# Kernel optimization log

Measured on AMD Instinct MI355X. Metric: run time of the kernel, lower is better.

The kernel has to match this reference:

```python
import jax, jax.numpy as jnp
import numpy as np

BLOCK_SIZE = 64
N_EMBD = 128
N_HEAD = 4
HEAD_DIM = N_EMBD // N_HEAD  # 32


def setup_inputs() -> dict:
    key = jax.random.key(0)
    kx, kq, kk, kv = jax.random.split(key, 4)
    B, T = 4096, 64
    x = jax.random.normal(kx, (B, T, N_EMBD), dtype=jnp.float32)
    # nn.Linear(n_embd, head_dim, bias=False): stored as [out,in] in torch,
    # here kept as [in, out] = [128, 32] so projection is x @ W.
    s = 1.0 / np.sqrt(N_EMBD)
    Wq = jax.random.uniform(kq, (N_EMBD, HEAD_DIM), jnp.float32, -s, s)
    Wk = jax.random.uniform(kk, (N_EMBD, HEAD_DIM), jnp.float32, -s, s)
    Wv = jax.random.uniform(kv, (N_EMBD, HEAD_DIM), jnp.float32, -s, s)
    return {"x": x, "Wq": Wq, "Wk": Wk, "Wv": Wv}


def reference(x, Wq, Wk, Wv):
    B, T, C = x.shape
    q = x @ Wq  # [B, T, Hd]
    k = x @ Wk
    v = x @ Wv
    scale = 1.0 / jnp.sqrt(jnp.asarray(k.shape[-1], x.dtype))
    wei = jnp.einsum("btd,bsd->bts", q, k) * scale  # [B, T, T]
    causal = jnp.tril(jnp.ones((T, T), dtype=bool))
    wei = jnp.where(causal, wei, -jnp.inf)
    wei = jax.nn.softmax(wei, axis=-1)
    out = jnp.einsum("bts,bsd->btd", wei, v)  # [B, T, Hd]
    return out
```

## Files before the change

kernel.cpp:

```cpp
#include <hip/hip_runtime.h>


#define TT 64
#define CC 128
#define HD 32

typedef __bf16 bf16_t;
typedef __bf16 bf8_t __attribute__((ext_vector_type(8)));
typedef __bf16 bf4_t __attribute__((ext_vector_type(4)));
typedef float  f4_t  __attribute__((ext_vector_type(4)));

__global__ __launch_bounds__(256) void prep_weights(
    const float* __restrict__ Wq, const float* __restrict__ Wk,
    const float* __restrict__ Wv, bf16_t* __restrict__ wf)
{
  int t = blockIdx.x * 256 + threadIdx.x;
  int j    = t & 7;
  int lane = (t >> 3) & 63;
  int kt   = (t >> 9) & 3;
  int n6   = t >> 11;
  int k    = kt * 32 + (lane >> 4) * 8 + j;
  int col  = (n6 & 1) * 16 + (lane & 15);
  const float* W = (n6 >> 1) == 0 ? Wq : ((n6 >> 1) == 1 ? Wk : Wv);
  wf[t] = (bf16_t)W[k * HD + col];
}

__global__ __launch_bounds__(256) void head_fused(
    const float* __restrict__ x, const bf8_t* __restrict__ wf,
    float* __restrict__ out)
{
  __shared__ __align__(16) bf16_t xs[TT][136];
  __shared__ __align__(16) bf16_t qs[TT][40];
  __shared__ __align__(16) bf16_t ks[TT][40];
  __shared__ __align__(16) bf16_t vt[HD][72];

  const int tid  = threadIdx.x;
  const int wave = tid >> 6;
  const int lane = tid & 63;
  const int quad = lane >> 4;
  const int l16  = lane & 15;
  const int b    = blockIdx.x;

  const float4* x4 = (const float4*)(x + (size_t)b * (TT * CC));
  #pragma unroll
  for (int i = 0; i < 8; ++i) {
    int e = tid + i * 256;
    float4 f = x4[e];
    int fi = e << 2;
    int row = fi >> 7, col = fi & 127;
    bf4_t h = { (bf16_t)f.x, (bf16_t)f.y, (bf16_t)f.z, (bf16_t)f.w };
    *(bf4_t*)&xs[row][col] = h;
  }
  __syncthreads();

  f4_t zero4 = {0.f, 0.f, 0.f, 0.f};
  f4_t acc[6];
  #pragma unroll
  for (int n = 0; n < 6; ++n) acc[n] = zero4;
  #pragma unroll
  for (int kk = 0; kk < 4; ++kk) {
    int k0 = kk * 32 + quad * 8;
    bf8_t a = *(const bf8_t*)&xs[wave * 16 + l16][k0];
    #pragma unroll
    for (int n = 0; n < 6; ++n) {
      bf8_t bb = wf[(n * 4 + kk) * 64 + lane];
      acc[n] = __builtin_amdgcn_mfma_f32_16x16x32_bf16(a, bb, acc[n], 0, 0, 0);
    }
  }
  #pragma unroll
  for (int r = 0; r < 4; ++r) {
    int row = wave * 16 + quad * 4 + r;
    qs[row][l16]      = (bf16_t)acc[0][r];
    qs[row][16 + l16] = (bf16_t)acc[1][r];
    ks[row][l16]      = (bf16_t)acc[2][r];
    ks[row][16 + l16] = (bf16_t)acc[3][r];
    vt[l16][row]      = (bf16_t)acc[4][r];
    vt[16 + l16][row] = (bf16_t)acc[5][r];
  }
  __syncthreads();

  bf16_t (*ps)[72] = (bf16_t(*)[72])&xs[0][0];
  f4_t sc[4];
  #pragma unroll
  for (int nt = 0; nt < 4; ++nt) sc[nt] = zero4;
  {
    bf8_t aq = *(const bf8_t*)&qs[wave * 16 + l16][quad * 8];
    #pragma unroll
    for (int nt = 0; nt < 4; ++nt) {
      if (nt <= wave) {
        bf8_t bk = *(const bf8_t*)&ks[nt * 16 + l16][quad * 8];
        sc[nt] = __builtin_amdgcn_mfma_f32_16x16x32_bf16(aq, bk, zero4, 0, 0, 0);
      }
    }
  }
  const float scale = 0.17677669529663687f;
  #pragma unroll
  for (int r = 0; r < 4; ++r) {
    int rl = quad * 4 + r;
    float vals[4];
    float vmax = -INFINITY;
    #pragma unroll
    for (int nt = 0; nt < 4; ++nt) {
      float v_ = -INFINITY;
      if (nt < wave)                         v_ = sc[nt][r] * scale;
      else if (nt == wave && l16 <= rl)      v_ = sc[nt][r] * scale;
      vals[nt] = v_;
      vmax = fmaxf(vmax, v_);
    }
    #pragma unroll
    for (int off = 1; off < 16; off <<= 1)
      vmax = fmaxf(vmax, __shfl_xor(vmax, off));
    float psum = 0.f;
    #pragma unroll
    for (int nt = 0; nt < 4; ++nt) {
      float p = (vals[nt] == -INFINITY) ? 0.f : __expf(vals[nt] - vmax);
      vals[nt] = p;
      psum += p;
    }
    #pragma unroll
    for (int off = 1; off < 16; off <<= 1)
      psum += __shfl_xor(psum, off);
    float inv = 1.0f / psum;
    int row = wave * 16 + rl;
    #pragma unroll
    for (int nt = 0; nt < 4; ++nt)
      ps[row][nt * 16 + l16] = (bf16_t)(vals[nt] * inv);
  }
  __syncthreads();

  f4_t o0 = zero4, o1 = zero4;
  #pragma unroll
  for (int kk = 0; kk < 2; ++kk) {
    int k0 = kk * 32 + quad * 8;
    bf8_t ap  = *(const bf8_t*)&ps[wave * 16 + l16][k0];
    bf8_t bv0 = *(const bf8_t*)&vt[l16][k0];
    bf8_t bv1 = *(const bf8_t*)&vt[16 + l16][k0];
    o0 = __builtin_amdgcn_mfma_f32_16x16x32_bf16(ap, bv0, o0, 0, 0, 0);
    o1 = __builtin_amdgcn_mfma_f32_16x16x32_bf16(ap, bv1, o1, 0, 0, 0);
  }
  float* ob = out + (size_t)b * (TT * HD);
  #pragma unroll
  for (int r = 0; r < 4; ++r) {
    int row = wave * 16 + quad * 4 + r;
    ob[row * HD + l16]      = o0[r];
    ob[row * HD + 16 + l16] = o1[r];
  }
}

extern "C" void kernel_launch(void* const* d_in, const int* in_sizes, int n_in,
                              void* d_out, int out_size, void* d_ws, size_t ws_size,
                              hipStream_t stream) {
  const float* x  = (const float*)d_in[0];
  const float* Wq = (const float*)d_in[1];
  const float* Wk = (const float*)d_in[2];
  const float* Wv = (const float*)d_in[3];
  float* out = (float*)d_out;
  bf16_t* wf = (bf16_t*)d_ws;
  int B = in_sizes[0] / (TT * CC);

  prep_weights<<<dim3(48), dim3(256), 0, stream>>>(Wq, Wk, Wv, wf);
  head_fused<<<dim3(B), dim3(256), 0, stream>>>(x, (const bf8_t*)wf, out);
}
```

Before: 219.0 us.

## Process each batch element with a single wave, removing block barriers

The attention kernel now runs one 64-thread wave per batch element instead of four waves. x is loaded straight from global memory into MFMA operand registers rather than staged through a shared-memory tile, and the softmax and PV stages loop over the four query row tiles in the same wave. This removes the __syncthreads barriers and the large x shared buffer, which allows more blocks per CU. In exchange each wave does four times the serial work, and the global x loads are strided per lane and less coalesced than before.

```diff
diff --git a/kernel.cpp b/kernel.cpp
--- a/kernel.cpp
+++ b/kernel.cpp
@@ -7,7 +7,6 @@
 
 typedef __bf16 bf16_t;
 typedef __bf16 bf8_t __attribute__((ext_vector_type(8)));
-typedef __bf16 bf4_t __attribute__((ext_vector_type(4)));
 typedef float  f4_t  __attribute__((ext_vector_type(4)));
 
 __global__ __launch_bounds__(256) void prep_weights(
@@ -25,125 +24,114 @@
   wf[t] = (bf16_t)W[k * HD + col];
 }
 
-__global__ __launch_bounds__(256) void head_fused(
+__global__ __launch_bounds__(64, 3) void head_fused(
     const float* __restrict__ x, const bf8_t* __restrict__ wf,
     float* __restrict__ out)
 {
-  __shared__ __align__(16) bf16_t xs[TT][136];
   __shared__ __align__(16) bf16_t qs[TT][40];
   __shared__ __align__(16) bf16_t ks[TT][40];
   __shared__ __align__(16) bf16_t vt[HD][72];
+  __shared__ __align__(16) bf16_t ps[16][72];
 
-  const int tid  = threadIdx.x;
-  const int wave = tid >> 6;
-  const int lane = tid & 63;
+  const int lane = threadIdx.x;
   const int quad = lane >> 4;
   const int l16  = lane & 15;
   const int b    = blockIdx.x;
+  const float* __restrict__ xb = x + (size_t)b * (TT * CC);
+  float* __restrict__ ob = out + (size_t)b * (TT * HD);
 
-  const float4* x4 = (const float4*)(x + (size_t)b * (TT * CC));
-  #pragma unroll
-  for (int i = 0; i < 8; ++i) {
-    int e = tid + i * 256;
-    float4 f = x4[e];
-    int fi = e << 2;
-    int row = fi >> 7, col = fi & 127;
-    bf4_t h = { (bf16_t)f.x, (bf16_t)f.y, (bf16_t)f.z, (bf16_t)f.w };
-    *(bf4_t*)&xs[row][col] = h;
-  }
-  __syncthreads();
+  const f4_t zero4 = {0.f, 0.f, 0.f, 0.f};
 
-  f4_t zero4 = {0.f, 0.f, 0.f, 0.f};
-  f4_t acc[6];
-  #pragma unroll
-  for (int n = 0; n < 6; ++n) acc[n] = zero4;
-  #pragma unroll
-  for (int kk = 0; kk < 4; ++kk) {
-    int k0 = kk * 32 + quad * 8;
-    bf8_t a = *(const bf8_t*)&xs[wave * 16 + l16][k0];
+  #pragma unroll 1
+  for (int i = 0; i < 4; ++i) {
+    f4_t acc[6];
     #pragma unroll
-    for (int n = 0; n < 6; ++n) {
-      bf8_t bb = wf[(n * 4 + kk) * 64 + lane];
-      acc[n] = __builtin_amdgcn_mfma_f32_16x16x32_bf16(a, bb, acc[n], 0, 0, 0);
+    for (int n = 0; n < 6; ++n) acc[n] = zero4;
+    #pragma unroll
+    for (int kk = 0; kk < 4; ++kk) {
+      const float* src = xb + (16 * i + l16) * CC + kk * 32 + quad * 8;
+      float4 f0 = *(const float4*)(src);
+      float4 f1 = *(const float4*)(src + 4);
+      bf8_t a;
+      a[0] = (bf16_t)f0.x; a[1] = (bf16_t)f0.y; a[2] = (bf16_t)f0.z; a[3] = (bf16_t)f0.w;
+      a[4] = (bf16_t)f1.x; a[5] = (bf16_t)f1.y; a[6] = (bf16_t)f1.z; a[7] = (bf16_t)f1.w;
+      #pragma unroll
+      for (int n = 0; n < 6; ++n) {
+        bf8_t bb = wf[(n * 4 + kk) * 64 + lane];
+        acc[n] = __builtin_amdgcn_mfma_f32_16x16x32_bf16(a, bb, acc[n], 0, 0, 0);
+      }
+    }
+    #pragma unroll
+    for (int r = 0; r < 4; ++r) {
+      int row = 16 * i + quad * 4 + r;
+      qs[row][l16]      = (bf16_t)acc[0][r];
+      qs[row][16 + l16] = (bf16_t)acc[1][r];
+      ks[row][l16]      = (bf16_t)acc[2][r];
+      ks[row][16 + l16] = (bf16_t)acc[3][r];
+      vt[l16][row]      = (bf16_t)acc[4][r];
+      vt[16 + l16][row] = (bf16_t)acc[5][r];
     }
   }
-  #pragma unroll
-  for (int r = 0; r < 4; ++r) {
-    int row = wave * 16 + quad * 4 + r;
-    qs[row][l16]      = (bf16_t)acc[0][r];
-    qs[row][16 + l16] = (bf16_t)acc[1][r];
-    ks[row][l16]      = (bf16_t)acc[2][r];
-    ks[row][16 + l16] = (bf16_t)acc[3][r];
-    vt[l16][row]      = (bf16_t)acc[4][r];
-    vt[16 + l16][row] = (bf16_t)acc[5][r];
-  }
-  __syncthreads();
 
-  bf16_t (*ps)[72] = (bf16_t(*)[72])&xs[0][0];
-  f4_t sc[4];
-  #pragma unroll
-  for (int nt = 0; nt < 4; ++nt) sc[nt] = zero4;
-  {
-    bf8_t aq = *(const bf8_t*)&qs[wave * 16 + l16][quad * 8];
+  const float scale = 0.17677669529663687f;
+  #pragma unroll 1
+  for (int i = 0; i < 4; ++i) {
+    f4_t sc[4];
+    bf8_t aq = *(const bf8_t*)&qs[16 * i + l16][quad * 8];
     #pragma unroll
-    for (int nt = 0; nt < 4; ++nt) {
-      if (nt <= wave) {
-        bf8_t bk = *(const bf8_t*)&ks[nt * 16 + l16][quad * 8];
-        sc[nt] = __builtin_amdgcn_mfma_f32_16x16x32_bf16(aq, bk, zero4, 0, 0, 0);
+    for (int j = 0; j < 4; ++j) {
+      sc[j] = zero4;
+      if (j <= i) {
+        bf8_t bk = *(const bf8_t*)&ks[16 * j + l16][quad * 8];
+        sc[j] = __builtin_amdgcn_mfma_f32_16x16x32_bf16(aq, bk, zero4, 0, 0, 0);
       }
     }
-  }
-  const float scale = 0.17677669529663687f;
-  #pragma unroll
-  for (int r = 0; r < 4; ++r) {
-    int rl = quad * 4 + r;
-    float vals[4];
-    float vmax = -INFINITY;
     #pragma unroll
-    for (int nt = 0; nt < 4; ++nt) {
-      float v_ = -INFINITY;
-      if (nt < wave)                         v_ = sc[nt][r] * scale;
-      else if (nt == wave && l16 <= rl)      v_ = sc[nt][r] * scale;
-      vals[nt] = v_;
-      vmax = fmaxf(vmax, v_);
+    for (int r = 0; r < 4; ++r) {
+      int rl = quad * 4 + r;
+      float vals[4];
+      float vmax = -INFINITY;
+      #pragma unroll
+      for (int j = 0; j < 4; ++j) {
+        bool valid = (j < i) | ((j == i) & (l16 <= rl));
+        float v_ = valid ? sc[j][r] * scale : -INFINITY;
+        vals[j] = v_;
+        vmax = fmaxf(vmax, v_);
+      }
+      #pragma unroll
+      for (int off = 1; off < 16; off <<= 1)
+        vmax = fmaxf(vmax, __shfl_xor(vmax, off));
+      float psum = 0.f;
+      #pragma unroll
+      for (int j = 0; j < 4; ++j) {
+        float p = (vals[j] == -INFINITY) ? 0.f : __expf(vals[j] - vmax);
+        vals[j] = p;
+        psum += p;
+      }
+      #pragma unroll
+      for (int off = 1; off < 16; off <<= 1)
+        psum += __shfl_xor(psum, off);
+      float inv = 1.0f / psum;
+      #pragma unroll
+      for (int j = 0; j < 4; ++j)
+        ps[rl][j * 16 + l16] = (bf16_t)(vals[j] * inv);
+    }
+    f4_t o0 = zero4, o1 = zero4;
+    #pragma unroll
+    for (int kk = 0; kk < 2; ++kk) {
+      int k0 = kk * 32 + quad * 8;
+      bf8_t ap  = *(const bf8_t*)&ps[l16][k0];
+      bf8_t bv0 = *(const bf8_t*)&vt[l16][k0];
+      bf8_t bv1 = *(const bf8_t*)&vt[16 + l16][k0];
+      o0 = __builtin_amdgcn_mfma_f32_16x16x32_bf16(ap, bv0, o0, 0, 0, 0);
+      o1 = __builtin_amdgcn_mfma_f32_16x16x32_bf16(ap, bv1, o1, 0, 0, 0);
     }
     #pragma unroll
-    for (int off = 1; off < 16; off <<= 1)
-      vmax = fmaxf(vmax, __shfl_xor(vmax, off));
-    float psum = 0.f;
-    #pragma unroll
-    for (int nt = 0; nt < 4; ++nt) {
-      float p = (vals[nt] == -INFINITY) ? 0.f : __expf(vals[nt] - vmax);
-      vals[nt] = p;
-      psum += p;
+    for (int r = 0; r < 4; ++r) {
+      int row = 16 * i + quad * 4 + r;
+      ob[row * HD + l16]      = o0[r];
+      ob[row * HD + 16 + l16] = o1[r];
     }
-    #pragma unroll
-    for (int off = 1; off < 16; off <<= 1)
-      psum += __shfl_xor(psum, off);
-    float inv = 1.0f / psum;
-    int row = wave * 16 + rl;
-    #pragma unroll
-    for (int nt = 0; nt < 4; ++nt)
-      ps[row][nt * 16 + l16] = (bf16_t)(vals[nt] * inv);
-  }
-  __syncthreads();
-
-  f4_t o0 = zero4, o1 = zero4;
-  #pragma unroll
-  for (int kk = 0; kk < 2; ++kk) {
-    int k0 = kk * 32 + quad * 8;
-    bf8_t ap  = *(const bf8_t*)&ps[wave * 16 + l16][k0];
-    bf8_t bv0 = *(const bf8_t*)&vt[l16][k0];
-    bf8_t bv1 = *(const bf8_t*)&vt[16 + l16][k0];
-    o0 = __builtin_amdgcn_mfma_f32_16x16x32_bf16(ap, bv0, o0, 0, 0, 0);
-    o1 = __builtin_amdgcn_mfma_f32_16x16x32_bf16(ap, bv1, o1, 0, 0, 0);
-  }
-  float* ob = out + (size_t)b * (TT * HD);
-  #pragma unroll
-  for (int r = 0; r < 4; ++r) {
-    int row = wave * 16 + quad * 4 + r;
-    ob[row * HD + l16]      = o0[r];
-    ob[row * HD + 16 + l16] = o1[r];
   }
 }
 
@@ -159,5 +147,5 @@
   int B = in_sizes[0] / (TT * CC);
 
   prep_weights<<<dim3(48), dim3(256), 0, stream>>>(Wq, Wk, Wv, wf);
-  head_fused<<<dim3(B), dim3(256), 0, stream>>>(x, (const bf8_t*)wf, out);
+  head_fused<<<dim3(B), dim3(64), 0, stream>>>(x, (const bf8_t*)wf, out);
 }
```

Result: no change. 218.4 us (-0.3%).
